# Optimization experiments

Hardware: AMD Instinct MI355X
Metric: run time of the kernel (lower is better)

## Reference

```python
import jax, jax.numpy as jnp
import numpy as np

B, N, E, D, AD = 8, 1000, 4, 64, 32  # batch, n_node, n_edge_types, state_dim, annotation_dim
W_SCALE = 0.02  # matches normal_(0.0, 0.02) init


def setup_inputs() -> dict:
    key = jax.random.key(0)
    ks = jax.random.split(key, 10)
    return {
        "prop_state": jax.random.normal(ks[0], (B, N, D), jnp.float32),
        "annotation": jax.random.normal(ks[1], (B, N, AD), jnp.float32),
        "A": jax.random.uniform(ks[2], (B, N, 2 * N * E), jnp.float32),
        "W_in": W_SCALE * jax.random.normal(ks[3], (E, D, D), jnp.float32),
        "W_out": W_SCALE * jax.random.normal(ks[4], (E, D, D), jnp.float32),
        "W_r": W_SCALE * jax.random.normal(ks[5], (D, 3 * D), jnp.float32),
        "W_z": W_SCALE * jax.random.normal(ks[6], (D, 3 * D), jnp.float32),
        "W_h": W_SCALE * jax.random.normal(ks[7], (D, 3 * D), jnp.float32),
        "Wo1": W_SCALE * jax.random.normal(ks[8], (D, D + AD), jnp.float32),
        "Wo2": W_SCALE * jax.random.normal(ks[9], (1, D), jnp.float32),
    }


def _propagate(state, A_in, A_out, W_in, W_out, W_r, W_z, W_h):
    b, n, d = state.shape
    e = W_in.shape[0]
    # per-edge-type linear transforms (torch Linear: y = x @ W.T), batched over edge types
    # layout matches torch: stack over e then transpose(0,1) -> [b, e, n, d] -> [b, e*n, d]
    s_in = jnp.einsum('bnd,efd->benf', state, W_in).reshape(b, e * n, d)
    s_out = jnp.einsum('bnd,efd->benf', state, W_out).reshape(b, e * n, d)
    a_in = jnp.matmul(A_in, s_in)    # [b, n, d]
    a_out = jnp.matmul(A_out, s_out)  # [b, n, d]
    a = jnp.concatenate([a_in, a_out, state], axis=2)  # [b, n, 3d]
    r = jax.nn.sigmoid(a @ W_r.T)
    z = jax.nn.sigmoid(a @ W_z.T)
    joined = jnp.concatenate([a_in, a_out, r * state], axis=2)
    h_hat = jnp.tanh(joined @ W_h.T)
    return (1.0 - z) * state + z * h_hat


def reference(prop_state, annotation, A, W_in, W_out, W_r, W_z, W_h, Wo1, Wo2):
    n = prop_state.shape[1]
    e = W_in.shape[0]
    ne = n * e
    A_in, A_out = A[:, :, :ne], A[:, :, ne:]
    # exactly two propagation steps (n_steps_flag path in the original)
    s1 = _propagate(prop_state, A_in, A_out, W_in, W_out, W_r, W_z, W_h)
    s2 = _propagate(s1, A_in, A_out, W_in, W_out, W_r, W_z, W_h)
    join_state = jnp.concatenate([s2, annotation], axis=2)  # [b, n, d+ad]
    out = jnp.tanh(join_state @ Wo1.T) @ Wo2.T  # [b, n, 1]
    return out.sum(axis=2)  # [b, n]
```

## Files before the change

### kernel.cpp

```cpp
#include <hip/hip_runtime.h>


typedef float  f32x4_t  __attribute__((ext_vector_type(4)));
typedef __bf16 bf16x8_t __attribute__((ext_vector_type(8)));
typedef __bf16 bf16x4_t __attribute__((ext_vector_type(4)));

#define MFMA16(a, b, c) __builtin_amdgcn_mfma_f32_16x16x32_bf16((a), (b), (c), 0, 0, 0)

static constexpr int kB  = 8;
static constexpr int kN  = 1000;
static constexpr int kD  = 64;
static constexpr int kAD = 32;
static constexpr int kNE = 4000;

__device__ __forceinline__ float4 ld4(const float* p) {
    return *reinterpret_cast<const float4*>(p);
}

__device__ __forceinline__ bf16x8_t cvt8(float4 a, float4 b) {
    bf16x8_t r;
    r[0] = (__bf16)a.x; r[1] = (__bf16)a.y; r[2] = (__bf16)a.z; r[3] = (__bf16)a.w;
    r[4] = (__bf16)b.x; r[5] = (__bf16)b.y; r[6] = (__bf16)b.z; r[7] = (__bf16)b.w;
    return r;
}

__device__ __forceinline__ float sigm(float x) {
    x = fminf(fmaxf(x, -30.f), 30.f);
    return 1.0f / (1.0f + __expf(-x));
}

__device__ __forceinline__ float fast_tanh(float x) {
    x = fminf(fmaxf(x, -15.f), 15.f);
    const float e = __expf(-2.0f * x);
    return (1.0f - e) / (1.0f + e);
}

__global__ __launch_bounds__(256) void precompute_swt(
    const float* __restrict__ state,
    const float* __restrict__ W_in,
    const float* __restrict__ W_out,
    __bf16* __restrict__ SWT)
{
    const int bx = blockIdx.x;
    const int jt = bx & 15;
    const int e  = (bx >> 4) & 3;
    const int h  = (bx >> 6) & 1;
    const int b  = bx >> 7;
    const float* W = (h ? W_out : W_in) + e * kD * kD;

    const int tid  = threadIdx.x;
    const int w    = tid >> 6;
    const int lane = tid & 63;
    const int m    = lane & 15;
    const int q    = lane >> 4;

    __shared__ __bf16 T[64][72];

    const int  jj    = jt * 64 + w * 16 + m;
    const bool valid = (jj < kN);
    const float* srow = state + ((size_t)b * kN + (valid ? jj : kN - 1)) * kD + q * 8;
    float4 a0 = ld4(srow),      a1 = ld4(srow + 4);
    float4 a2 = ld4(srow + 32), a3 = ld4(srow + 36);
    if (!valid) {
        a0 = make_float4(0.f, 0.f, 0.f, 0.f); a1 = a0; a2 = a0; a3 = a0;
    }
    const bf16x8_t af0 = cvt8(a0, a1);
    const bf16x8_t af1 = cvt8(a2, a3);

    #pragma unroll
    for (int c = 0; c < 4; ++c) {
        const int f = c * 16 + m;
        const float* wrow = W + f * kD + q * 8;
        const bf16x8_t bf0 = cvt8(ld4(wrow),      ld4(wrow + 4));
        const bf16x8_t bf1 = cvt8(ld4(wrow + 32), ld4(wrow + 36));
        f32x4_t acc = {0.f, 0.f, 0.f, 0.f};
        acc = MFMA16(af0, bf0, acc);
        acc = MFMA16(af1, bf1, acc);
        const int j0 = w * 16 + q * 4;
        bf16x4_t v;
        v[0] = (__bf16)acc[0]; v[1] = (__bf16)acc[1];
        v[2] = (__bf16)acc[2]; v[3] = (__bf16)acc[3];
        *reinterpret_cast<bf16x4_t*>(&T[f][j0]) = v;
    }
    __syncthreads();

    const size_t rowbase = (size_t)((b * 2 + h) * kD);
    #pragma unroll
    for (int rep = 0; rep < 2; ++rep) {
        const int cc = tid + rep * 256;
        const int f  = cc >> 3;
        const int ch = cc & 7;
        const int jj0 = jt * 64 + ch * 8;
        if (jj0 < kN) {
            const uint4 v = *reinterpret_cast<uint4*>(&T[f][ch * 8]);
            *reinterpret_cast<uint4*>(SWT + (rowbase + f) * kNE + e * kN + jj0) = v;
        }
    }
}

__global__ __launch_bounds__(256) void big_mm(
    const float* __restrict__ A,
    const __bf16* __restrict__ SWT,
    float* __restrict__ a_in,
    float* __restrict__ a_out)
{
    const int bx   = blockIdx.x;
    const int tile = bx & 15;
    const int h    = (bx >> 4) & 1;
    const int b    = bx >> 5;
    const int tid  = threadIdx.x;
    const int w    = tid >> 6;
    const int lane = tid & 63;
    const int m    = lane & 15;
    const int q    = lane >> 4;

    const int row  = tile * 64 + w * 16 + m;
    const int rowc = row < kN ? row : kN - 1;

    const float*  Ap = A + ((size_t)b * kN + rowc) * (2 * kNE) + h * kNE + q * 8;
    const __bf16* SW = SWT + ((size_t)(b * 2 + h) * kD) * kNE + q * 8;
    const __bf16* SB0 = SW + (size_t)(0 * 16 + m) * kNE;
    const __bf16* SB1 = SW + (size_t)(1 * 16 + m) * kNE;
    const __bf16* SB2 = SW + (size_t)(2 * 16 + m) * kNE;
    const __bf16* SB3 = SW + (size_t)(3 * 16 + m) * kNE;

    f32x4_t acc0 = {0.f, 0.f, 0.f, 0.f};
    f32x4_t acc1 = {0.f, 0.f, 0.f, 0.f};
    f32x4_t acc2 = {0.f, 0.f, 0.f, 0.f};
    f32x4_t acc3 = {0.f, 0.f, 0.f, 0.f};

    bf16x8_t ca0 = cvt8(ld4(Ap + 0),  ld4(Ap + 4));
    bf16x8_t ca1 = cvt8(ld4(Ap + 32), ld4(Ap + 36));
    bf16x8_t cb00 = *(const bf16x8_t*)(SB0);
    bf16x8_t cb01 = *(const bf16x8_t*)(SB1);
    bf16x8_t cb02 = *(const bf16x8_t*)(SB2);
    bf16x8_t cb03 = *(const bf16x8_t*)(SB3);
    bf16x8_t cb10 = *(const bf16x8_t*)(SB0 + 32);
    bf16x8_t cb11 = *(const bf16x8_t*)(SB1 + 32);
    bf16x8_t cb12 = *(const bf16x8_t*)(SB2 + 32);
    bf16x8_t cb13 = *(const bf16x8_t*)(SB3 + 32);

    for (int kk = 0; kk < 62; ++kk) {
        const int kn = (kk + 1) * 64;
        const int k2 = (kk < 61) ? (kn + 32) : 0;

        const float4 x0 = ld4(Ap + kn),  x1 = ld4(Ap + kn + 4);
        const float4 x2 = ld4(Ap + k2),  x3 = ld4(Ap + k2 + 4);
        const bf16x8_t nb00 = *(const bf16x8_t*)(SB0 + kn);
        const bf16x8_t nb01 = *(const bf16x8_t*)(SB1 + kn);
        const bf16x8_t nb02 = *(const bf16x8_t*)(SB2 + kn);
        const bf16x8_t nb03 = *(const bf16x8_t*)(SB3 + kn);
        const bf16x8_t nb10 = *(const bf16x8_t*)(SB0 + k2);
        const bf16x8_t nb11 = *(const bf16x8_t*)(SB1 + k2);
        const bf16x8_t nb12 = *(const bf16x8_t*)(SB2 + k2);
        const bf16x8_t nb13 = *(const bf16x8_t*)(SB3 + k2);

        acc0 = MFMA16(ca0, cb00, acc0);
        acc1 = MFMA16(ca0, cb01, acc1);
        acc2 = MFMA16(ca0, cb02, acc2);
        acc3 = MFMA16(ca0, cb03, acc3);
        acc0 = MFMA16(ca1, cb10, acc0);
        acc1 = MFMA16(ca1, cb11, acc1);
        acc2 = MFMA16(ca1, cb12, acc2);
        acc3 = MFMA16(ca1, cb13, acc3);

        ca0 = cvt8(x0, x1);
        ca1 = cvt8(x2, x3);
        cb00 = nb00; cb01 = nb01; cb02 = nb02; cb03 = nb03;
        cb10 = nb10; cb11 = nb11; cb12 = nb12; cb13 = nb13;
    }
    acc0 = MFMA16(ca0, cb00, acc0);
    acc1 = MFMA16(ca0, cb01, acc1);
    acc2 = MFMA16(ca0, cb02, acc2);
    acc3 = MFMA16(ca0, cb03, acc3);

    float* dst = (h ? a_out : a_in) + (size_t)b * kN * kD;
    const int i0 = tile * 64 + w * 16 + q * 4;
    #pragma unroll
    for (int r = 0; r < 4; ++r) {
        const int i = i0 + r;
        if (i < kN) {
            float* drow = dst + (size_t)i * kD + m;
            drow[0]  = acc0[r];
            drow[16] = acc1[r];
            drow[32] = acc2[r];
            drow[48] = acc3[r];
        }
    }
}

__global__ __launch_bounds__(64) void gating(
    const float* __restrict__ a_in,
    const float* __restrict__ a_out,
    const float* __restrict__ state,
    const float* __restrict__ W_r,
    const float* __restrict__ W_z,
    const float* __restrict__ W_h,
    float* __restrict__ s_next,
    const float* __restrict__ ann,
    const float* __restrict__ Wo1,
    const float* __restrict__ Wo2,
    float* __restrict__ out,
    const int step)
{
    const int i0   = blockIdx.x * 16;
    const int lane = threadIdx.x;
    const int m    = lane & 15;
    const int q    = lane >> 4;

    __shared__ __bf16 TL[16][72];

    const size_t rowA = (size_t)(i0 + m);

    bf16x8_t xf[6];
    {
        const float* p = a_in + rowA * kD + q * 8;
        xf[0] = cvt8(ld4(p),      ld4(p + 4));
        xf[1] = cvt8(ld4(p + 32), ld4(p + 36));
        p = a_out + rowA * kD + q * 8;
        xf[2] = cvt8(ld4(p),      ld4(p + 4));
        xf[3] = cvt8(ld4(p + 32), ld4(p + 36));
        p = state + rowA * kD + q * 8;
        xf[4] = cvt8(ld4(p),      ld4(p + 4));
        xf[5] = cvt8(ld4(p + 32), ld4(p + 36));
    }

    f32x4_t accr[4], accz[4], acch[4];
    #pragma unroll
    for (int c = 0; c < 4; ++c) {
        accr[c] = {0.f, 0.f, 0.f, 0.f};
        accz[c] = {0.f, 0.f, 0.f, 0.f};
        acch[c] = {0.f, 0.f, 0.f, 0.f};
    }

    #pragma unroll
    for (int c = 0; c < 4; ++c) {
        const int f = c * 16 + m;
        const float* wr = W_r + f * 192 + q * 8;
        const float* wz = W_z + f * 192 + q * 8;
        const float* wh = W_h + f * 192 + q * 8;
        #pragma unroll
        for (int kc = 0; kc < 6; ++kc) {
            bf16x8_t bw;
            bw = cvt8(ld4(wr + kc * 32), ld4(wr + kc * 32 + 4));
            accr[c] = MFMA16(xf[kc], bw, accr[c]);
            bw = cvt8(ld4(wz + kc * 32), ld4(wz + kc * 32 + 4));
            accz[c] = MFMA16(xf[kc], bw, accz[c]);
            if (kc < 4) {
                bw = cvt8(ld4(wh + kc * 32), ld4(wh + kc * 32 + 4));
                acch[c] = MFMA16(xf[kc], bw, acch[c]);
            }
        }
    }

    float sC[4][4];
    #pragma unroll
    for (int c = 0; c < 4; ++c)
        #pragma unroll
        for (int r = 0; r < 4; ++r)
            sC[c][r] = state[(size_t)(i0 + q * 4 + r) * kD + c * 16 + m];

    #pragma unroll
    for (int c = 0; c < 4; ++c)
        #pragma unroll
        for (int r = 0; r < 4; ++r)
            TL[q * 4 + r][c * 16 + m] = (__bf16)(sigm(accr[c][r]) * sC[c][r]);
    __syncthreads();
    const bf16x8_t rs0 = *(const bf16x8_t*)&TL[m][q * 8];
    const bf16x8_t rs1 = *(const bf16x8_t*)&TL[m][32 + q * 8];

    #pragma unroll
    for (int c = 0; c < 4; ++c) {
        const int f = c * 16 + m;
        const float* wh3 = W_h + f * 192 + 128 + q * 8;
        acch[c] = MFMA16(rs0, cvt8(ld4(wh3),      ld4(wh3 + 4)),  acch[c]);
        acch[c] = MFMA16(rs1, cvt8(ld4(wh3 + 32), ld4(wh3 + 36)), acch[c]);
    }

    float ns[4][4];
    #pragma unroll
    for (int c = 0; c < 4; ++c)
        #pragma unroll
        for (int r = 0; r < 4; ++r) {
            const float zv = sigm(accz[c][r]);
            const float hv = fast_tanh(acch[c][r]);
            ns[c][r] = (1.f - zv) * sC[c][r] + zv * hv;
        }

    if (step == 1) {
        #pragma unroll
        for (int c = 0; c < 4; ++c)
            #pragma unroll
            for (int r = 0; r < 4; ++r)
                s_next[(size_t)(i0 + q * 4 + r) * kD + c * 16 + m] = ns[c][r];
    } else {
        __syncthreads();
        #pragma unroll
        for (int c = 0; c < 4; ++c)
            #pragma unroll
            for (int r = 0; r < 4; ++r)
                TL[q * 4 + r][c * 16 + m] = (__bf16)ns[c][r];
        __syncthreads();
        const bf16x8_t j0 = *(const bf16x8_t*)&TL[m][q * 8];
        const bf16x8_t j1 = *(const bf16x8_t*)&TL[m][32 + q * 8];
        const float* ap = ann + rowA * kAD + q * 8;
        const bf16x8_t j2 = cvt8(ld4(ap), ld4(ap + 4));

        f32x4_t acco[4];
        #pragma unroll
        for (int c = 0; c < 4; ++c) acco[c] = {0.f, 0.f, 0.f, 0.f};
        #pragma unroll
        for (int c = 0; c < 4; ++c) {
            const float* wo = Wo1 + (size_t)(c * 16 + m) * 96 + q * 8;
            acco[c] = MFMA16(j0, cvt8(ld4(wo),      ld4(wo + 4)),  acco[c]);
            acco[c] = MFMA16(j1, cvt8(ld4(wo + 32), ld4(wo + 36)), acco[c]);
            acco[c] = MFMA16(j2, cvt8(ld4(wo + 64), ld4(wo + 68)), acco[c]);
        }
        float vs[4] = {0.f, 0.f, 0.f, 0.f};
        #pragma unroll
        for (int c = 0; c < 4; ++c) {
            const float w2 = Wo2[c * 16 + m];
            #pragma unroll
            for (int r = 0; r < 4; ++r)
                vs[r] += fast_tanh(acco[c][r]) * w2;
        }
        #pragma unroll
        for (int off = 1; off <= 8; off <<= 1) {
            #pragma unroll
            for (int r = 0; r < 4; ++r)
                vs[r] += __shfl_xor(vs[r], off, 64);
        }
        if (m == 0) {
            #pragma unroll
            for (int r = 0; r < 4; ++r)
                out[i0 + q * 4 + r] = vs[r];
        }
    }
}

extern "C" void kernel_launch(void* const* d_in, const int* in_sizes, int n_in,
                              void* d_out, int out_size, void* d_ws, size_t ws_size,
                              hipStream_t stream) {
    (void)in_sizes; (void)n_in; (void)out_size; (void)ws_size;

    const float* prop_state = (const float*)d_in[0];
    const float* annotation = (const float*)d_in[1];
    const float* A          = (const float*)d_in[2];
    const float* W_in       = (const float*)d_in[3];
    const float* W_out      = (const float*)d_in[4];
    const float* W_r        = (const float*)d_in[5];
    const float* W_z        = (const float*)d_in[6];
    const float* W_h        = (const float*)d_in[7];
    const float* Wo1        = (const float*)d_in[8];
    const float* Wo2        = (const float*)d_in[9];
    float* out = (float*)d_out;

    char* ws = (char*)d_ws;
    __bf16* SWT  = (__bf16*)(ws);
    float*  a_in = (float*)(ws + 8192000);
    float*  a_out= (float*)(ws + 10240000);
    float*  s1   = (float*)(ws + 12288000);

    precompute_swt<<<1024, 256, 0, stream>>>(prop_state, W_in, W_out, SWT);
    big_mm<<<256, 256, 0, stream>>>(A, SWT, a_in, a_out);
    gating<<<500, 64, 0, stream>>>(a_in, a_out, prop_state, W_r, W_z, W_h,
                                   s1, nullptr, nullptr, nullptr, nullptr, 1);
    precompute_swt<<<1024, 256, 0, stream>>>(s1, W_in, W_out, SWT);
    big_mm<<<256, 256, 0, stream>>>(A, SWT, a_in, a_out);
    gating<<<500, 64, 0, stream>>>(a_in, a_out, s1, W_r, W_z, W_h,
                                   nullptr, annotation, Wo1, Wo2, out, 2);
}
```

Before: 531.3 us.

## Split big_mm K dimension across two blocks and widen gating to four waves

```diff
diff --git a/kernel.cpp b/kernel.cpp
--- a/kernel.cpp
+++ b/kernel.cpp
@@ -12,15 +12,33 @@
 static constexpr int kD  = 64;
 static constexpr int kAD = 32;
 static constexpr int kNE = 4000;
+static constexpr int kBN = 8000;
+static constexpr int kP  = kBN * kD;
 
 __device__ __forceinline__ float4 ld4(const float* p) {
     return *reinterpret_cast<const float4*>(p);
+}
+
+__device__ __forceinline__ float4 ldnt4(const float* p) {
+    const f32x4_t v = __builtin_nontemporal_load(reinterpret_cast<const f32x4_t*>(p));
+    return make_float4(v.x, v.y, v.z, v.w);
 }
 
 __device__ __forceinline__ bf16x8_t cvt8(float4 a, float4 b) {
     bf16x8_t r;
     r[0] = (__bf16)a.x; r[1] = (__bf16)a.y; r[2] = (__bf16)a.z; r[3] = (__bf16)a.w;
     r[4] = (__bf16)b.x; r[5] = (__bf16)b.y; r[6] = (__bf16)b.z; r[7] = (__bf16)b.w;
+    return r;
+}
+
+__device__ __forceinline__ bf16x8_t sum8(const float* p0, const float* p1) {
+    const float4 a0 = ld4(p0), a1 = ld4(p0 + 4);
+    const float4 b0 = ld4(p1), b1 = ld4(p1 + 4);
+    bf16x8_t r;
+    r[0] = (__bf16)(a0.x + b0.x); r[1] = (__bf16)(a0.y + b0.y);
+    r[2] = (__bf16)(a0.z + b0.z); r[3] = (__bf16)(a0.w + b0.w);
+    r[4] = (__bf16)(a1.x + b1.x); r[5] = (__bf16)(a1.y + b1.y);
+    r[6] = (__bf16)(a1.z + b1.z); r[7] = (__bf16)(a1.w + b1.w);
     return r;
 }
 
@@ -98,16 +116,17 @@
     }
 }
 
-__global__ __launch_bounds__(256) void big_mm(
+__global__ __launch_bounds__(256, 2) void big_mm(
     const float* __restrict__ A,
     const __bf16* __restrict__ SWT,
-    float* __restrict__ a_in,
-    float* __restrict__ a_out)
+    float* __restrict__ a_in_p,
+    float* __restrict__ a_out_p)
 {
     const int bx   = blockIdx.x;
     const int tile = bx & 15;
     const int h    = (bx >> 4) & 1;
-    const int b    = bx >> 5;
+    const int b    = (bx >> 5) & 7;
+    const int ks   = (bx >> 8) & 1;
     const int tid  = threadIdx.x;
     const int w    = tid >> 6;
     const int lane = tid & 63;
@@ -116,9 +135,10 @@
 
     const int row  = tile * 64 + w * 16 + m;
     const int rowc = row < kN ? row : kN - 1;
-
-    const float*  Ap = A + ((size_t)b * kN + rowc) * (2 * kNE) + h * kNE + q * 8;
-    const __bf16* SW = SWT + ((size_t)(b * 2 + h) * kD) * kNE + q * 8;
+    const int kbeg = ks * 1984;
+
+    const float*  Ap = A + ((size_t)b * kN + rowc) * (2 * kNE) + h * kNE + kbeg + q * 8;
+    const __bf16* SW = SWT + ((size_t)(b * 2 + h) * kD) * kNE + kbeg + q * 8;
     const __bf16* SB0 = SW + (size_t)(0 * 16 + m) * kNE;
     const __bf16* SB1 = SW + (size_t)(1 * 16 + m) * kNE;
     const __bf16* SB2 = SW + (size_t)(2 * 16 + m) * kNE;
@@ -129,8 +149,8 @@
     f32x4_t acc2 = {0.f, 0.f, 0.f, 0.f};
     f32x4_t acc3 = {0.f, 0.f, 0.f, 0.f};
 
-    bf16x8_t ca0 = cvt8(ld4(Ap + 0),  ld4(Ap + 4));
-    bf16x8_t ca1 = cvt8(ld4(Ap + 32), ld4(Ap + 36));
+    bf16x8_t ca0 = cvt8(ldnt4(Ap + 0),  ldnt4(Ap + 4));
+    bf16x8_t ca1 = cvt8(ldnt4(Ap + 32), ldnt4(Ap + 36));
     bf16x8_t cb00 = *(const bf16x8_t*)(SB0);
     bf16x8_t cb01 = *(const bf16x8_t*)(SB1);
     bf16x8_t cb02 = *(const bf16x8_t*)(SB2);
@@ -140,12 +160,12 @@
     bf16x8_t cb12 = *(const bf16x8_t*)(SB2 + 32);
     bf16x8_t cb13 = *(const bf16x8_t*)(SB3 + 32);
 
-    for (int kk = 0; kk < 62; ++kk) {
+    for (int kk = 0; kk < 31; ++kk) {
         const int kn = (kk + 1) * 64;
-        const int k2 = (kk < 61) ? (kn + 32) : 0;
-
-        const float4 x0 = ld4(Ap + kn),  x1 = ld4(Ap + kn + 4);
-        const float4 x2 = ld4(Ap + k2),  x3 = ld4(Ap + k2 + 4);
+        const int k2 = (kk < 30) ? (kn + 32) : 0;
+
+        const float4 x0 = ldnt4(Ap + kn),  x1 = ldnt4(Ap + kn + 4);
+        const float4 x2 = ldnt4(Ap + k2),  x3 = ldnt4(Ap + k2 + 4);
         const bf16x8_t nb00 = *(const bf16x8_t*)(SB0 + kn);
         const bf16x8_t nb01 = *(const bf16x8_t*)(SB1 + kn);
         const bf16x8_t nb02 = *(const bf16x8_t*)(SB2 + kn);
@@ -169,12 +189,14 @@
         cb00 = nb00; cb01 = nb01; cb02 = nb02; cb03 = nb03;
         cb10 = nb10; cb11 = nb11; cb12 = nb12; cb13 = nb13;
     }
-    acc0 = MFMA16(ca0, cb00, acc0);
-    acc1 = MFMA16(ca0, cb01, acc1);
-    acc2 = MFMA16(ca0, cb02, acc2);
-    acc3 = MFMA16(ca0, cb03, acc3);
-
-    float* dst = (h ? a_out : a_in) + (size_t)b * kN * kD;
+    if (ks == 1) {
+        acc0 = MFMA16(ca0, cb00, acc0);
+        acc1 = MFMA16(ca0, cb01, acc1);
+        acc2 = MFMA16(ca0, cb02, acc2);
+        acc3 = MFMA16(ca0, cb03, acc3);
+    }
+
+    float* dst = (h ? a_out_p : a_in_p) + (size_t)ks * kP + (size_t)b * kN * kD;
     const int i0 = tile * 64 + w * 16 + q * 4;
     #pragma unroll
     for (int r = 0; r < 4; ++r) {
@@ -189,9 +211,9 @@
     }
 }
 
-__global__ __launch_bounds__(64) void gating(
-    const float* __restrict__ a_in,
-    const float* __restrict__ a_out,
+__global__ __launch_bounds__(256, 2) void gating(
+    const float* __restrict__ a_in_p,
+    const float* __restrict__ a_out_p,
     const float* __restrict__ state,
     const float* __restrict__ W_r,
     const float* __restrict__ W_z,
@@ -204,126 +226,95 @@
     const int step)
 {
     const int i0   = blockIdx.x * 16;
-    const int lane = threadIdx.x;
+    const int tid  = threadIdx.x;
+    const int c    = tid >> 6;
+    const int lane = tid & 63;
     const int m    = lane & 15;
     const int q    = lane >> 4;
+    const int f    = c * 16 + m;
 
     __shared__ __bf16 TL[16][72];
+    __shared__ float  Osum[4][16];
 
     const size_t rowA = (size_t)(i0 + m);
 
     bf16x8_t xf[6];
     {
-        const float* p = a_in + rowA * kD + q * 8;
-        xf[0] = cvt8(ld4(p),      ld4(p + 4));
-        xf[1] = cvt8(ld4(p + 32), ld4(p + 36));
-        p = a_out + rowA * kD + q * 8;
-        xf[2] = cvt8(ld4(p),      ld4(p + 4));
-        xf[3] = cvt8(ld4(p + 32), ld4(p + 36));
+        const float* p = a_in_p + rowA * kD + q * 8;
+        xf[0] = sum8(p,      p + kP);
+        xf[1] = sum8(p + 32, p + 32 + kP);
+        p = a_out_p + rowA * kD + q * 8;
+        xf[2] = sum8(p,      p + kP);
+        xf[3] = sum8(p + 32, p + 32 + kP);
         p = state + rowA * kD + q * 8;
         xf[4] = cvt8(ld4(p),      ld4(p + 4));
         xf[5] = cvt8(ld4(p + 32), ld4(p + 36));
     }
 
-    f32x4_t accr[4], accz[4], acch[4];
-    #pragma unroll
-    for (int c = 0; c < 4; ++c) {
-        accr[c] = {0.f, 0.f, 0.f, 0.f};
-        accz[c] = {0.f, 0.f, 0.f, 0.f};
-        acch[c] = {0.f, 0.f, 0.f, 0.f};
-    }
-
-    #pragma unroll
-    for (int c = 0; c < 4; ++c) {
-        const int f = c * 16 + m;
-        const float* wr = W_r + f * 192 + q * 8;
-        const float* wz = W_z + f * 192 + q * 8;
-        const float* wh = W_h + f * 192 + q * 8;
-        #pragma unroll
-        for (int kc = 0; kc < 6; ++kc) {
-            bf16x8_t bw;
-            bw = cvt8(ld4(wr + kc * 32), ld4(wr + kc * 32 + 4));
-            accr[c] = MFMA16(xf[kc], bw, accr[c]);
-            bw = cvt8(ld4(wz + kc * 32), ld4(wz + kc * 32 + 4));
-            accz[c] = MFMA16(xf[kc], bw, accz[c]);
-            if (kc < 4) {
-                bw = cvt8(ld4(wh + kc * 32), ld4(wh + kc * 32 + 4));
-                acch[c] = MFMA16(xf[kc], bw, acch[c]);
-            }
-        }
-    }
-
-    float sC[4][4];
-    #pragma unroll
-    for (int c = 0; c < 4; ++c)
-        #pragma unroll
-        for (int r = 0; r < 4; ++r)
-            sC[c][r] = state[(size_t)(i0 + q * 4 + r) * kD + c * 16 + m];
-
-    #pragma unroll
-    for (int c = 0; c < 4; ++c)
-        #pragma unroll
-        for (int r = 0; r < 4; ++r)
-            TL[q * 4 + r][c * 16 + m] = (__bf16)(sigm(accr[c][r]) * sC[c][r]);
+    f32x4_t accr = {0.f, 0.f, 0.f, 0.f};
+    f32x4_t accz = {0.f, 0.f, 0.f, 0.f};
+    f32x4_t acch = {0.f, 0.f, 0.f, 0.f};
+
+    const float* wr = W_r + f * 192 + q * 8;
+    const float* wz = W_z + f * 192 + q * 8;
+    const float* wh = W_h + f * 192 + q * 8;
+    #pragma unroll
+    for (int kc = 0; kc < 6; ++kc) {
+        accr = MFMA16(xf[kc], cvt8(ld4(wr + kc * 32), ld4(wr + kc * 32 + 4)), accr);
+        accz = MFMA16(xf[kc], cvt8(ld4(wz + kc * 32), ld4(wz + kc * 32 + 4)), accz);
+        if (kc < 4)
+            acch = MFMA16(xf[kc], cvt8(ld4(wh + kc * 32), ld4(wh + kc * 32 + 4)), acch);
+    }
+
+    float sC[4];
+    #pragma unroll
+    for (int r = 0; r < 4; ++r)
+        sC[r] = state[(size_t)(i0 + q * 4 + r) * kD + f];
+
+    #pragma unroll
+    for (int r = 0; r < 4; ++r)
+        TL[q * 4 + r][f] = (__bf16)(sigm(accr[r]) * sC[r]);
     __syncthreads();
     const bf16x8_t rs0 = *(const bf16x8_t*)&TL[m][q * 8];
     const bf16x8_t rs1 = *(const bf16x8_t*)&TL[m][32 + q * 8];
 
-    #pragma unroll
-    for (int c = 0; c < 4; ++c) {
-        const int f = c * 16 + m;
-        const float* wh3 = W_h + f * 192 + 128 + q * 8;
-        acch[c] = MFMA16(rs0, cvt8(ld4(wh3),      ld4(wh3 + 4)),  acch[c]);
-        acch[c] = MFMA16(rs1, cvt8(ld4(wh3 + 32), ld4(wh3 + 36)), acch[c]);
-    }
-
-    float ns[4][4];
-    #pragma unroll
-    for (int c = 0; c < 4; ++c)
-        #pragma unroll
-        for (int r = 0; r < 4; ++r) {
-            const float zv = sigm(accz[c][r]);
-            const float hv = fast_tanh(acch[c][r]);
-            ns[c][r] = (1.f - zv) * sC[c][r] + zv * hv;
-        }
+    const float* wh3 = W_h + f * 192 + 128 + q * 8;
+    acch = MFMA16(rs0, cvt8(ld4(wh3),      ld4(wh3 + 4)),  acch);
+    acch = MFMA16(rs1, cvt8(ld4(wh3 + 32), ld4(wh3 + 36)), acch);
+
+    float ns[4];
+    #pragma unroll
+    for (int r = 0; r < 4; ++r) {
+        const float zv = sigm(accz[r]);
+        ns[r] = (1.f - zv) * sC[r] + zv * fast_tanh(acch[r]);
+    }
 
     if (step == 1) {
         #pragma unroll
-        for (int c = 0; c < 4; ++c)
-            #pragma unroll
-            for (int r = 0; r < 4; ++r)
-                s_next[(size_t)(i0 + q * 4 + r) * kD + c * 16 + m] = ns[c][r];
+        for (int r = 0; r < 4; ++r)
+            s_next[(size_t)(i0 + q * 4 + r) * kD + f] = ns[r];
     } else {
         __syncthreads();
         #pragma unroll
-        for (int c = 0; c < 4; ++c)
-            #pragma unroll
-            for (int r = 0; r < 4; ++r)
-                TL[q * 4 + r][c * 16 + m] = (__bf16)ns[c][r];
+        for (int r = 0; r < 4; ++r)
+            TL[q * 4 + r][f] = (__bf16)ns[r];
         __syncthreads();
         const bf16x8_t j0 = *(const bf16x8_t*)&TL[m][q * 8];
         const bf16x8_t j1 = *(const bf16x8_t*)&TL[m][32 + q * 8];
         const float* ap = ann + rowA * kAD + q * 8;
         const bf16x8_t j2 = cvt8(ld4(ap), ld4(ap + 4));
 
-        f32x4_t acco[4];
+        f32x4_t acco = {0.f, 0.f, 0.f, 0.f};
+        const float* wo = Wo1 + (size_t)f * 96 + q * 8;
+        acco = MFMA16(j0, cvt8(ld4(wo),      ld4(wo + 4)),  acco);
+        acco = MFMA16(j1, cvt8(ld4(wo + 32), ld4(wo + 36)), acco);
+        acco = MFMA16(j2, cvt8(ld4(wo + 64), ld4(wo + 68)), acco);
+
+        const float w2 = Wo2[f];
+        float vs[4];
         #pragma unroll
-        for (int c = 0; c < 4; ++c) acco[c] = {0.f, 0.f, 0.f, 0.f};
-        #pragma unroll
-        for (int c = 0; c < 4; ++c) {
-            const float* wo = Wo1 + (size_t)(c * 16 + m) * 96 + q * 8;
-            acco[c] = MFMA16(j0, cvt8(ld4(wo),      ld4(wo + 4)),  acco[c]);
-            acco[c] = MFMA16(j1, cvt8(ld4(wo + 32), ld4(wo + 36)), acco[c]);
-            acco[c] = MFMA16(j2, cvt8(ld4(wo + 64), ld4(wo + 68)), acco[c]);
-        }
-        float vs[4] = {0.f, 0.f, 0.f, 0.f};
-        #pragma unroll
-        for (int c = 0; c < 4; ++c) {
-            const float w2 = Wo2[c * 16 + m];
-            #pragma unroll
-            for (int r = 0; r < 4; ++r)
-                vs[r] += fast_tanh(acco[c][r]) * w2;
-        }
+        for (int r = 0; r < 4; ++r)
+            vs[r] = fast_tanh(acco[r]) * w2;
         #pragma unroll
         for (int off = 1; off <= 8; off <<= 1) {
             #pragma unroll
@@ -333,8 +324,11 @@
         if (m == 0) {
             #pragma unroll
             for (int r = 0; r < 4; ++r)
-                out[i0 + q * 4 + r] = vs[r];
+                Osum[c][q * 4 + r] = vs[r];
         }
+        __syncthreads();
+        if (tid < 16)
+            out[i0 + tid] = Osum[0][tid] + Osum[1][tid] + Osum[2][tid] + Osum[3][tid];
     }
 }
 
@@ -356,17 +350,17 @@
     float* out = (float*)d_out;
 
     char* ws = (char*)d_ws;
-    __bf16* SWT  = (__bf16*)(ws);
-    float*  a_in = (float*)(ws + 8192000);
-    float*  a_out= (float*)(ws + 10240000);
-    float*  s1   = (float*)(ws + 12288000);
+    __bf16* SWT    = (__bf16*)(ws);
+    float*  a_in_p = (float*)(ws + 8192000);
+    float*  a_out_p= (float*)(ws + 12288000);
+    float*  s1     = (float*)(ws + 16384000);
 
     precompute_swt<<<1024, 256, 0, stream>>>(prop_state, W_in, W_out, SWT);
-    big_mm<<<256, 256, 0, stream>>>(A, SWT, a_in, a_out);
-    gating<<<500, 64, 0, stream>>>(a_in, a_out, prop_state, W_r, W_z, W_h,
-                                   s1, nullptr, nullptr, nullptr, nullptr, 1);
+    big_mm<<<512, 256, 0, stream>>>(A, SWT, a_in_p, a_out_p);
+    gating<<<500, 256, 0, stream>>>(a_in_p, a_out_p, prop_state, W_r, W_z, W_h,
+                                    s1, nullptr, nullptr, nullptr, nullptr, 1);
     precompute_swt<<<1024, 256, 0, stream>>>(s1, W_in, W_out, SWT);
-    big_mm<<<256, 256, 0, stream>>>(A, SWT, a_in, a_out);
-    gating<<<500, 64, 0, stream>>>(a_in, a_out, s1, W_r, W_z, W_h,
-                                   nullptr, annotation, Wo1, Wo2, out, 2);
-}
+    big_mm<<<512, 256, 0, stream>>>(A, SWT, a_in_p, a_out_p);
+    gating<<<500, 256, 0, stream>>>(a_in_p, a_out_p, s1, W_r, W_z, W_h,
+                                    nullptr, annotation, Wo1, Wo2, out, 2);
+}
```

Result: slower. 549.4 us (+3.4%).
